# Performance work log

Hardware: AMD Instinct MI355X
Metric: run time of the kernel (lower is better)

The kernel has to match this reference:

```python
import jax, jax.numpy as jnp
import numpy as np

B, T, HID = 2, 2048, 1536
H, HKV, D = 12, 2, 128
EPS = 1e-6
NEG = -1e9


def setup_inputs() -> dict:
    key = jax.random.key(0)
    ks = jax.random.split(key, 8)
    # rotary embeddings built from real angles (cos/sin of position*inv_freq)
    inv_freq = 1.0 / (10000.0 ** (jnp.arange(0, D, 2, dtype=jnp.float32) / D))  # [D/2]
    pos = jnp.arange(T, dtype=jnp.float32)
    ang = pos[:, None] * inv_freq[None, :]                       # [T, D/2]
    emb = jnp.concatenate([ang, ang], axis=-1)                   # [T, D]
    cos = jnp.broadcast_to(jnp.cos(emb)[None], (B, T, D))
    sin = jnp.broadcast_to(jnp.sin(emb)[None], (B, T, D))
    # additive causal mask [1,1,T,T]
    causal = jnp.tril(jnp.ones((T, T), dtype=bool))
    attention_mask = jnp.where(causal, 0.0, NEG).astype(jnp.float32)[None, None]
    s = 0.02
    return {
        "hidden_states": jax.random.normal(ks[0], (B, T, HID), jnp.float32),
        "cos": cos,
        "sin": sin,
        "attention_mask": attention_mask,
        "q_w": jax.random.normal(ks[1], (H * D, HID), jnp.float32) * s,
        "k_w": jax.random.normal(ks[2], (HKV * D, HID), jnp.float32) * s,
        "v_w": jax.random.normal(ks[3], (HKV * D, HID), jnp.float32) * s,
        "o_w": jax.random.normal(ks[4], (HID, H * D), jnp.float32) * s,
        "q_norm_w": jnp.ones((D,), jnp.float32),
        "k_norm_w": jnp.ones((D,), jnp.float32),
    }


def _rms_norm(x, w):
    # per-head RMSNorm over last dim (head_dim), computed in fp32
    xf = x.astype(jnp.float32)
    var = jnp.mean(xf * xf, axis=-1, keepdims=True)
    return (w * (xf * jax.lax.rsqrt(var + EPS))).astype(x.dtype)


def _rotate_half(x):
    x1, x2 = jnp.split(x, 2, axis=-1)
    return jnp.concatenate([-x2, x1], axis=-1)


def reference(hidden_states, cos, sin, attention_mask, q_w, k_w, v_w, o_w, q_norm_w, k_norm_w):
    b, t, _ = hidden_states.shape
    n_rep = H // HKV
    scale = D ** -0.5

    # projections -> [B, n_heads, T, D]
    q = (hidden_states @ q_w.T).reshape(b, t, H, D)
    k = (hidden_states @ k_w.T).reshape(b, t, HKV, D)
    v = (hidden_states @ v_w.T).reshape(b, t, HKV, D).transpose(0, 2, 1, 3)

    # per-head QK RMSNorm, then to [B, H, T, D]
    q = _rms_norm(q, q_norm_w).transpose(0, 2, 1, 3)
    k = _rms_norm(k, k_norm_w).transpose(0, 2, 1, 3)

    # RoPE (cos/sin broadcast over head axis)
    c = cos[:, None, :, :]
    s = sin[:, None, :, :]
    q = q * c + _rotate_half(q) * s
    k = k * c + _rotate_half(k) * s

    # GQA repeat_kv: [B, HKV, T, D] -> [B, H, T, D]
    k = jnp.repeat(k, n_rep, axis=1)
    v = jnp.repeat(v, n_rep, axis=1)

    attn = jnp.einsum('bhqd,bhkd->bhqk', q, k) * scale + attention_mask
    attn = jax.nn.softmax(attn.astype(jnp.float32), axis=-1).astype(q.dtype)
    out = jnp.einsum('bhqk,bhkd->bhqd', attn, v)
    out = out.transpose(0, 2, 1, 3).reshape(b, t, H * D)
    return out @ o_w.T
```

## Files before the change

### kernel.cpp

```cpp
#include <hip/hip_runtime.h>
#include <hip/hip_bf16.h>


#define B_   2
#define T_   2048
#define HID_ 1536
#define H_   12
#define HKV_ 2
#define D_   128
#define GQ_  (H_ / HKV_)
#define NQKV_ 2048
#define SCALE_ 0.08838834764831845f

typedef unsigned short u16;
typedef __attribute__((ext_vector_type(4))) float f32x4;
typedef __attribute__((ext_vector_type(8))) short bf16x8;
typedef __attribute__((ext_vector_type(4))) unsigned short u16x4;
typedef __attribute__((ext_vector_type(8))) unsigned short u16x8;

__device__ __forceinline__ u16 f2b(float f) {
  union { __hip_bfloat16 h; u16 u; } cv;
  cv.h = __float2bfloat16(f);
  return cv.u;
}
__device__ __forceinline__ float b2f(u16 u) {
  union { float f; unsigned i; } cv;
  cv.i = ((unsigned)u) << 16;
  return cv.f;
}

__device__ __forceinline__ void glds16(const u16* g, u16* l) {
  __builtin_amdgcn_global_load_lds((const __attribute__((address_space(1))) void*)g,
                                   (__attribute__((address_space(3))) void*)l, 16, 0, 0);
}

__global__ __launch_bounds__(256) void cvt_f32_bf16(const float* __restrict__ src,
                                                    u16* __restrict__ dst, int n4) {
  int i = blockIdx.x * 256 + threadIdx.x;
  const int stride = gridDim.x * 256;
  for (; i < n4; i += stride) {
    const float4 v = reinterpret_cast<const float4*>(src)[i];
    u16x4 o = {f2b(v.x), f2b(v.y), f2b(v.z), f2b(v.w)};
    reinterpret_cast<u16x4*>(dst)[i] = o;
  }
}

__device__ __forceinline__ void cstore(float* p, float v) { *p = v; }
__device__ __forceinline__ void cstore(u16* p, float v) { *p = f2b(v); }

template <typename CT>
__global__ __launch_bounds__(256) void gemm_bt(const u16* __restrict__ A,
                                               const u16* __restrict__ W,
                                               CT* __restrict__ C,
                                               int M, int N, int K) {
  __shared__ __align__(16) u16 As[128 * 32];
  __shared__ __align__(16) u16 Ws[128 * 32];
  const int tid  = threadIdx.x;
  const int lane = tid & 63;
  const int wid  = tid >> 6;
  const int wr = wid >> 1, wc = wid & 1;
  const int l15 = lane & 15, kg = lane >> 4;
  const int rowBase = blockIdx.y * 128;
  const int colBase = blockIdx.x * 128;

  const int srow = lane >> 2;
  const int scol = (lane & 3) << 3;
  const u16* Ab = A + (size_t)(rowBase + wid * 16 + srow) * K + scol;
  const u16* Wb = W + (size_t)(colBase + wid * 16 + srow) * K + scol;
  u16* AsW = &As[wid * 512];
  u16* WsW = &Ws[wid * 512];

  const f32x4 zero4 = {0.f, 0.f, 0.f, 0.f};
  f32x4 acc[4][4];
#pragma unroll
  for (int m = 0; m < 4; ++m)
#pragma unroll
    for (int n = 0; n < 4; ++n) acc[m][n] = zero4;

  for (int k0 = 0; k0 < K; k0 += 32) {
    __syncthreads();
    glds16(Ab + k0, AsW);
    glds16(Ab + (size_t)64 * K + k0, AsW + 2048);
    glds16(Wb + k0, WsW);
    glds16(Wb + (size_t)64 * K + k0, WsW + 2048);
    __syncthreads();
    bf16x8 a[4], b[4];
#pragma unroll
    for (int m = 0; m < 4; ++m)
      a[m] = *reinterpret_cast<const bf16x8*>(&As[(wr * 64 + m * 16 + l15) * 32 + kg * 8]);
#pragma unroll
    for (int n = 0; n < 4; ++n)
      b[n] = *reinterpret_cast<const bf16x8*>(&Ws[(wc * 64 + n * 16 + l15) * 32 + kg * 8]);
#pragma unroll
    for (int m = 0; m < 4; ++m)
#pragma unroll
      for (int n = 0; n < 4; ++n)
        acc[m][n] = __builtin_amdgcn_mfma_f32_16x16x32_bf16(a[m], b[n], acc[m][n], 0, 0, 0);
  }
#pragma unroll
  for (int m = 0; m < 4; ++m) {
    const int row0 = rowBase + wr * 64 + m * 16 + kg * 4;
#pragma unroll
    for (int n = 0; n < 4; ++n) {
      const int col = colBase + wc * 64 + n * 16 + l15;
#pragma unroll
      for (int r = 0; r < 4; ++r) cstore(&C[(size_t)(row0 + r) * N + col], acc[m][n][r]);
    }
  }
}

__global__ __launch_bounds__(256) void norm_rope_cvt(
    const u16* __restrict__ qkv, const float* __restrict__ cosb,
    const float* __restrict__ sinb, const float* __restrict__ q_nw,
    const float* __restrict__ k_nw, u16* __restrict__ q_b,
    u16* __restrict__ k_b, u16* __restrict__ vt_b) {
  const int gwave = (int)((blockIdx.x * 256 + threadIdx.x) >> 6);
  const int lane = threadIdx.x & 63;
  const int NQ = B_ * T_ * H_;
  const int NK = B_ * T_ * HKV_;
  if (gwave < NQ) {
    const int bt = gwave / H_, h = gwave - bt * H_;
    const u16* src = qkv + (size_t)bt * NQKV_ + h * D_;
    const float x1 = b2f(src[lane]), x2 = b2f(src[lane + 64]);
    float ss = x1 * x1 + x2 * x2;
#pragma unroll
    for (int m = 32; m >= 1; m >>= 1) ss += __shfl_xor(ss, m);
    const float rinv = rsqrtf(ss * (1.0f / D_) + 1e-6f);
    const float c1 = cosb[(size_t)bt * D_ + lane], c2 = cosb[(size_t)bt * D_ + lane + 64];
    const float s1 = sinb[(size_t)bt * D_ + lane], s2 = sinb[(size_t)bt * D_ + lane + 64];
    const float n1 = x1 * rinv * q_nw[lane], n2 = x2 * rinv * q_nw[lane + 64];
    const float o1 = (n1 * c1 - n2 * s1) * SCALE_;
    const float o2 = (n2 * c2 + n1 * s2) * SCALE_;
    const int b = bt >> 11, t = bt & (T_ - 1);
    u16* dst = q_b + ((size_t)(b * H_ + h) * T_ + t) * D_;
    dst[lane] = f2b(o1);
    dst[lane + 64] = f2b(o2);
  } else if (gwave < NQ + NK) {
    const int r = gwave - NQ;
    const int bt = r >> 1, hv = r & 1;
    const u16* src = qkv + (size_t)bt * NQKV_ + 1536 + hv * D_;
    const float x1 = b2f(src[lane]), x2 = b2f(src[lane + 64]);
    float ss = x1 * x1 + x2 * x2;
#pragma unroll
    for (int m = 32; m >= 1; m >>= 1) ss += __shfl_xor(ss, m);
    const float rinv = rsqrtf(ss * (1.0f / D_) + 1e-6f);
    const float c1 = cosb[(size_t)bt * D_ + lane], c2 = cosb[(size_t)bt * D_ + lane + 64];
    const float s1 = sinb[(size_t)bt * D_ + lane], s2 = sinb[(size_t)bt * D_ + lane + 64];
    const float n1 = x1 * rinv * k_nw[lane], n2 = x2 * rinv * k_nw[lane + 64];
    const float o1 = n1 * c1 - n2 * s1;
    const float o2 = n2 * c2 + n1 * s2;
    const int b = bt >> 11, t = bt & (T_ - 1);
    u16* dst = k_b + ((size_t)(b * HKV_ + hv) * T_ + t) * D_;
    dst[lane] = f2b(o1);
    dst[lane + 64] = f2b(o2);
  } else {
    const int r = gwave - NQ - NK;
    const int bt = r >> 1, hv = r & 1;
    const u16* src = qkv + (size_t)bt * NQKV_ + 1792 + hv * D_;
    const float x1 = b2f(src[lane]), x2 = b2f(src[lane + 64]);
    const int b = bt >> 11, t = bt & (T_ - 1);
    u16* dst = vt_b + (size_t)(b * HKV_ + hv) * D_ * T_;
    dst[(size_t)lane * T_ + t] = f2b(x1);
    dst[(size_t)(lane + 64) * T_ + t] = f2b(x2);
  }
}

__global__ __launch_bounds__(256) void attn_kernel(const u16* __restrict__ q_b,
                                                   const u16* __restrict__ k_b,
                                                   const u16* __restrict__ vt_b,
                                                   u16* __restrict__ aout,
                                                   u16* __restrict__ po0,
                                                   float2* __restrict__ ml) {
  __shared__ __align__(16) u16 Ks[64 * 128];
  __shared__ __align__(16) u16 Vs[64 * 128];
  __shared__ __align__(16) u16 P_lds[64][80];
  const int bh = blockIdx.x;
  const int y = blockIdx.y;
  const int qt = (y < 32) ? y : y - 16;
  const int s = (y < 32) ? 0 : 1;
  const int kt0 = s * 16;
  const int ktend = (s == 0) ? min(qt, 15) : qt;
  const bool splitq = (qt >= 16);
  const int b = bh / H_, h = bh - b * H_;
  const int kvh = h / GQ_;
  const int tid = threadIdx.x;
  const int w = tid >> 6, lane = tid & 63;
  const int l15 = lane & 15, kg = lane >> 4;
  const int qbase = qt * 64;

  const u16* Kb = k_b + (size_t)(b * HKV_ + kvh) * T_ * D_;
  const u16* Vb = vt_b + (size_t)(b * HKV_ + kvh) * D_ * T_;

  const u16* qrow = q_b + ((size_t)(b * H_ + h) * T_ + qbase + w * 16 + l15) * D_;
  bf16x8 qf[4];
#pragma unroll
  for (int ss = 0; ss < 4; ++ss)
    qf[ss] = *reinterpret_cast<const bf16x8*>(qrow + ss * 32 + kg * 8);

  const int krow0 = tid >> 4;
  const int kcol8 = (tid & 15) << 3;
  const int kdst0 = krow0 * 128 + (kcol8 ^ (krow0 << 3));
  const u16* ksrc0 = Kb + (size_t)krow0 * D_ + kcol8;

  const int vd0 = tid >> 3;
  const int vkk0 = (tid & 7) << 3;
  const int vdst0 = (vd0 >> 1) * 128 + ((((vd0 & 1) << 6) | vkk0) ^ ((vd0 >> 1) << 3));
  const u16* vsrc0 = Vb + (size_t)vd0 * T_ + vkk0;

  int koff[4];
#pragma unroll
  for (int ss = 0; ss < 4; ++ss) koff[ss] = (ss * 32 + kg * 8) ^ (l15 << 3);
  const int kbase = l15 * 128;
  int voff[2][2];
#pragma unroll
  for (int p = 0; p < 2; ++p)
#pragma unroll
    for (int ks = 0; ks < 2; ++ks)
      voff[p][ks] = (((l15 & 1) << 6) | (ks * 32) | (kg * 8)) ^ (((p << 3) | (l15 >> 1)) << 3);
  const int vrowb = (l15 >> 1) * 128;

  u16x8 kpre[4], vpre[4];
#pragma unroll
  for (int c = 0; c < 4; ++c) {
    kpre[c] = *reinterpret_cast<const u16x8*>(ksrc0 + (size_t)kt0 * 64 * D_ + c * 2048);
    vpre[c] = *reinterpret_cast<const u16x8*>(vsrc0 + (size_t)kt0 * 64 + (size_t)c * 32 * T_);
  }

  const f32x4 zero4 = {0.f, 0.f, 0.f, 0.f};
  f32x4 o[8];
#pragma unroll
  for (int n = 0; n < 8; ++n) o[n] = zero4;
  float mrow[4] = {-3e38f, -3e38f, -3e38f, -3e38f};
  float lsum[4] = {0.f, 0.f, 0.f, 0.f};

  for (int kt = kt0; kt <= ktend; ++kt) {
    __syncthreads();
#pragma unroll
    for (int c = 0; c < 4; ++c) {
      *reinterpret_cast<u16x8*>(&Ks[kdst0 + c * 2048]) = kpre[c];
      *reinterpret_cast<u16x8*>(&Vs[vdst0 + c * 2048]) = vpre[c];
    }
    __syncthreads();
    if (kt < ktend) {
      const size_t kadv = (size_t)(kt + 1) * 64;
#pragma unroll
      for (int c = 0; c < 4; ++c) {
        kpre[c] = *reinterpret_cast<const u16x8*>(ksrc0 + kadv * D_ + c * 2048);
        vpre[c] = *reinterpret_cast<const u16x8*>(vsrc0 + kadv + (size_t)c * 32 * T_);
      }
    }
    f32x4 sc[4];
#pragma unroll
    for (int n = 0; n < 4; ++n) sc[n] = zero4;
#pragma unroll
    for (int n = 0; n < 4; ++n)
#pragma unroll
      for (int ss = 0; ss < 4; ++ss) {
        bf16x8 kf = *reinterpret_cast<const bf16x8*>(&Ks[n * 2048 + kbase + koff[ss]]);
        sc[n] = __builtin_amdgcn_mfma_f32_16x16x32_bf16(qf[ss], kf, sc[n], 0, 0, 0);
      }
    if (kt == qt) {
#pragma unroll
      for (int n = 0; n < 4; ++n)
#pragma unroll
        for (int r = 0; r < 4; ++r)
          if (n * 16 + l15 > w * 16 + kg * 4 + r) sc[n][r] = -3e38f;
    }
    float pmax[4];
#pragma unroll
    for (int r = 0; r < 4; ++r) {
      float v = fmaxf(fmaxf(sc[0][r], sc[1][r]), fmaxf(sc[2][r], sc[3][r]));
      v = fmaxf(v, __shfl_xor(v, 1));
      v = fmaxf(v, __shfl_xor(v, 2));
      v = fmaxf(v, __shfl_xor(v, 4));
      v = fmaxf(v, __shfl_xor(v, 8));
      pmax[r] = v;
    }
    const bool grow = (pmax[0] > mrow[0] + 8.f) | (pmax[1] > mrow[1] + 8.f) |
                      (pmax[2] > mrow[2] + 8.f) | (pmax[3] > mrow[3] + 8.f);
    if (__any(grow)) {
#pragma unroll
      for (int r = 0; r < 4; ++r) {
        const float mnew = fmaxf(mrow[r], pmax[r]);
        const float alpha = __expf(mrow[r] - mnew);
        mrow[r] = mnew;
        lsum[r] *= alpha;
#pragma unroll
        for (int n = 0; n < 8; ++n) o[n][r] *= alpha;
      }
    }
    float rs[4] = {0.f, 0.f, 0.f, 0.f};
#pragma unroll
    for (int n = 0; n < 4; ++n)
#pragma unroll
      for (int r = 0; r < 4; ++r) {
        const float p = __expf(sc[n][r] - mrow[r]);
        rs[r] += p;
        P_lds[w * 16 + kg * 4 + r][n * 16 + l15] = f2b(p);
      }
#pragma unroll
    for (int r = 0; r < 4; ++r) {
      float v = rs[r];
      v += __shfl_xor(v, 1);
      v += __shfl_xor(v, 2);
      v += __shfl_xor(v, 4);
      v += __shfl_xor(v, 8);
      lsum[r] += v;
    }
#pragma unroll
    for (int ks = 0; ks < 2; ++ks) {
      bf16x8 pf = *reinterpret_cast<const bf16x8*>(&P_lds[w * 16 + l15][ks * 32 + kg * 8]);
#pragma unroll
      for (int n = 0; n < 8; ++n) {
        bf16x8 vf = *reinterpret_cast<const bf16x8*>(&Vs[n * 1024 + vrowb + voff[n & 1][ks]]);
        o[n] = __builtin_amdgcn_mfma_f32_16x16x32_bf16(pf, vf, o[n], 0, 0, 0);
      }
    }
  }

  const int t0 = qbase + w * 16 + kg * 4;
  if (!splitq) {
    float inv[4];
#pragma unroll
    for (int r = 0; r < 4; ++r) inv[r] = 1.0f / lsum[r];
#pragma unroll
    for (int n = 0; n < 8; ++n)
#pragma unroll
      for (int r = 0; r < 4; ++r)
        aout[(size_t)(b * T_ + t0 + r) * (H_ * D_) + h * D_ + n * 16 + l15] =
            f2b(o[n][r] * inv[r]);
  } else {
    const int slot = (bh << 4) + (qt - 16);
    if (l15 == 0) {
#pragma unroll
      for (int r = 0; r < 4; ++r) {
        const int row = w * 16 + kg * 4 + r;
        float2 v; v.x = mrow[r]; v.y = lsum[r];
        ml[(size_t)(slot * 2 + s) * 64 + row] = v;
      }
    }
    if (s == 1) {
#pragma unroll
      for (int n = 0; n < 8; ++n)
#pragma unroll
        for (int r = 0; r < 4; ++r)
          aout[(size_t)(b * T_ + t0 + r) * (H_ * D_) + h * D_ + n * 16 + l15] =
              f2b(o[n][r]);
    } else {
#pragma unroll
      for (int n = 0; n < 8; ++n)
#pragma unroll
        for (int r = 0; r < 4; ++r)
          po0[((size_t)slot * 64 + w * 16 + kg * 4 + r) * 128 + n * 16 + l15] =
              f2b(o[n][r]);
    }
  }
}

__global__ __launch_bounds__(256) void combine_kernel(u16* __restrict__ aout,
                                                      const u16* __restrict__ po0,
                                                      const float2* __restrict__ ml) {
  const int bh = blockIdx.x;
  const int qt16 = blockIdx.y;
  const int slot = (bh << 4) + qt16;
  const int b = bh / H_, h = bh - b * H_;
  const int t0 = (qt16 + 16) * 64;
  const int tid = threadIdx.x;
  const int row = tid >> 2;
  const int colc = (tid & 3) << 5;

  const float2 ml0 = ml[(size_t)(slot * 2 + 0) * 64 + row];
  const float2 ml1 = ml[(size_t)(slot * 2 + 1) * 64 + row];
  const float m = fmaxf(ml0.x, ml1.x);
  const float c0 = __expf(ml0.x - m), c1 = __expf(ml1.x - m);
  const float inv = 1.0f / (ml0.y * c0 + ml1.y * c1);
  const float s0 = c0 * inv, s1 = c1 * inv;

  const u16* p0 = po0 + ((size_t)slot * 64 + row) * 128 + colc;
  u16* a = aout + (size_t)(b * T_ + t0 + row) * (H_ * D_) + h * D_ + colc;
#pragma unroll
  for (int j = 0; j < 4; ++j) {
    u16x8 v0 = *reinterpret_cast<const u16x8*>(p0 + j * 8);
    u16x8 v1 = *reinterpret_cast<const u16x8*>(a + j * 8);
    u16x8 out;
#pragma unroll
    for (int e = 0; e < 8; ++e) out[e] = f2b(b2f(v0[e]) * s0 + b2f(v1[e]) * s1);
    *reinterpret_cast<u16x8*>(a + j * 8) = out;
  }
}

extern "C" void kernel_launch(void* const* d_in, const int* in_sizes, int n_in,
                              void* d_out, int out_size, void* d_ws, size_t ws_size,
                              hipStream_t stream) {
  const float* hidden = (const float*)d_in[0];
  const float* cosb   = (const float*)d_in[1];
  const float* sinb   = (const float*)d_in[2];
  const float* q_w  = (const float*)d_in[4];
  const float* k_w  = (const float*)d_in[5];
  const float* v_w  = (const float*)d_in[6];
  const float* o_w  = (const float*)d_in[7];
  const float* q_nw = (const float*)d_in[8];
  const float* k_nw = (const float*)d_in[9];
  float* out = (float*)d_out;

  char* ws = (char*)d_ws;
  const size_t MB = 1u << 20;
  u16*    hidden_b = (u16*)(ws);
  u16*    qkvw     = (u16*)(ws + 12 * MB);
  u16*    q_b      = (u16*)(ws);
  u16*    aout     = (u16*)(ws + 12 * MB);
  float2* ml       = (float2*)(ws + 24 * MB);
  u16*    k_b      = (u16*)(ws + 24 * MB + 512 * 1024);
  u16*    vt_b     = (u16*)(ws + 26 * MB + 512 * 1024);
  u16*    owb      = (u16*)(ws + 28 * MB + 512 * 1024);
  u16*    qkv_proj = (u16*)d_out;
  u16*    po0      = (u16*)d_out;

  const dim3 blk(256);
  const int M = B_ * T_;

  {
    const int nh = (B_ * T_ * HID_) / 4;
    const int nq = (H_ * D_ * HID_) / 4;
    const int nk = (HKV_ * D_ * HID_) / 4;
    cvt_f32_bf16<<<2048, blk, 0, stream>>>(hidden, hidden_b, nh);
    cvt_f32_bf16<<<2048, blk, 0, stream>>>(q_w, qkvw, nq);
    cvt_f32_bf16<<<384, blk, 0, stream>>>(k_w, qkvw + (size_t)1536 * HID_, nk);
    cvt_f32_bf16<<<384, blk, 0, stream>>>(v_w, qkvw + (size_t)1792 * HID_, nk);
    cvt_f32_bf16<<<2048, blk, 0, stream>>>(o_w, owb, nq);
  }

  gemm_bt<u16><<<dim3(NQKV_ / 128, M / 128), blk, 0, stream>>>(hidden_b, qkvw, qkv_proj,
                                                               M, NQKV_, HID_);

  norm_rope_cvt<<<16384, blk, 0, stream>>>(qkv_proj, cosb, sinb, q_nw, k_nw,
                                           q_b, k_b, vt_b);

  attn_kernel<<<dim3(B_ * H_, 48), blk, 0, stream>>>(q_b, k_b, vt_b, aout, po0, ml);
  combine_kernel<<<dim3(B_ * H_, 16), blk, 0, stream>>>(aout, po0, ml);

  gemm_bt<float><<<dim3(HID_ / 128, M / 128), blk, 0, stream>>>(aout, owb, out,
                                                                M, HID_, HID_);
}
```

Before: 216.1 us.

## Restructure attention to 128-row Q tiles with transposed QK and async double-buffered K/V

The attention kernel now processes 128 query rows per block, with each wave holding two 16-row Q sub-tiles, so every K/V fragment read from LDS feeds two MFMAs. S is computed transposed (K as the A operand), which lets P be packed into registers directly and removes the P round-trip through shared memory. K/V tiles are loaded with direct global-to-LDS copies into a double buffer, and V is written in a permuted token order so it matches the MFMA layout. Grid and combine sizes are halved to match. This adds register pressure and lowers the block count, and glds16 must already exist in the hidden part of the code.

```diff
diff --git a/kernel.cpp b/kernel.cpp
--- a/kernel.cpp
+++ b/kernel.cpp
@@ -159,9 +159,12 @@
     const u16* src = qkv + (size_t)bt * NQKV_ + 1792 + hv * D_;
     const float x1 = b2f(src[lane]), x2 = b2f(src[lane + 64]);
     const int b = bt >> 11, t = bt & (T_ - 1);
+    const int kk = t & 63;
+    const int tp = (t & ~63) | (kk & 32) | (((kk >> 2) & 3) << 3) |
+                   (((kk >> 4) & 1) << 2) | (kk & 3);
     u16* dst = vt_b + (size_t)(b * HKV_ + hv) * D_ * T_;
-    dst[(size_t)lane * T_ + t] = f2b(x1);
-    dst[(size_t)(lane + 64) * T_ + t] = f2b(x2);
+    dst[(size_t)lane * T_ + tp] = f2b(x1);
+    dst[(size_t)(lane + 64) * T_ + tp] = f2b(x2);
   }
 }
 
@@ -171,188 +174,227 @@
                                                    u16* __restrict__ aout,
                                                    u16* __restrict__ po0,
                                                    float2* __restrict__ ml) {
-  __shared__ __align__(16) u16 Ks[64 * 128];
-  __shared__ __align__(16) u16 Vs[64 * 128];
-  __shared__ __align__(16) u16 P_lds[64][80];
+  __shared__ __align__(16) u16 Ks[2][64 * 128];
+  __shared__ __align__(16) u16 Vs[2][128 * 64];
   const int bh = blockIdx.x;
   const int y = blockIdx.y;
-  const int qt = (y < 32) ? y : y - 16;
-  const int s = (y < 32) ? 0 : 1;
+  const int qt = (y < 16) ? y : (y - 8);
+  const int s = (y < 16) ? 0 : 1;
   const int kt0 = s * 16;
-  const int ktend = (s == 0) ? min(qt, 15) : qt;
-  const bool splitq = (qt >= 16);
+  const int ktend = (s == 0) ? min(2 * qt + 1, 15) : (2 * qt + 1);
+  const bool splitq = (qt >= 8);
   const int b = bh / H_, h = bh - b * H_;
   const int kvh = h / GQ_;
   const int tid = threadIdx.x;
   const int w = tid >> 6, lane = tid & 63;
   const int l15 = lane & 15, kg = lane >> 4;
-  const int qbase = qt * 64;
+  const int qbase = qt * 128;
 
   const u16* Kb = k_b + (size_t)(b * HKV_ + kvh) * T_ * D_;
   const u16* Vb = vt_b + (size_t)(b * HKV_ + kvh) * D_ * T_;
 
-  const u16* qrow = q_b + ((size_t)(b * H_ + h) * T_ + qbase + w * 16 + l15) * D_;
-  bf16x8 qf[4];
-#pragma unroll
-  for (int ss = 0; ss < 4; ++ss)
-    qf[ss] = *reinterpret_cast<const bf16x8*>(qrow + ss * 32 + kg * 8);
-
-  const int krow0 = tid >> 4;
-  const int kcol8 = (tid & 15) << 3;
-  const int kdst0 = krow0 * 128 + (kcol8 ^ (krow0 << 3));
-  const u16* ksrc0 = Kb + (size_t)krow0 * D_ + kcol8;
-
-  const int vd0 = tid >> 3;
-  const int vkk0 = (tid & 7) << 3;
-  const int vdst0 = (vd0 >> 1) * 128 + ((((vd0 & 1) << 6) | vkk0) ^ ((vd0 >> 1) << 3));
-  const u16* vsrc0 = Vb + (size_t)vd0 * T_ + vkk0;
-
-  int koff[4];
-#pragma unroll
-  for (int ss = 0; ss < 4; ++ss) koff[ss] = (ss * 32 + kg * 8) ^ (l15 << 3);
-  const int kbase = l15 * 128;
-  int voff[2][2];
-#pragma unroll
-  for (int p = 0; p < 2; ++p)
-#pragma unroll
-    for (int ks = 0; ks < 2; ++ks)
-      voff[p][ks] = (((l15 & 1) << 6) | (ks * 32) | (kg * 8)) ^ (((p << 3) | (l15 >> 1)) << 3);
-  const int vrowb = (l15 >> 1) * 128;
-
-  u16x8 kpre[4], vpre[4];
+  bf16x8 qf[2][4];
+#pragma unroll
+  for (int qb = 0; qb < 2; ++qb) {
+    const u16* qrow =
+        q_b + ((size_t)(b * H_ + h) * T_ + qbase + w * 32 + qb * 16 + l15) * D_;
+#pragma unroll
+    for (int s4 = 0; s4 < 4; ++s4)
+      qf[qb][s4] = *reinterpret_cast<const bf16x8*>(qrow + s4 * 32 + kg * 8);
+  }
+
+  int kK[4], vK[4];
 #pragma unroll
   for (int c = 0; c < 4; ++c) {
-    kpre[c] = *reinterpret_cast<const u16x8*>(ksrc0 + (size_t)kt0 * 64 * D_ + c * 2048);
-    vpre[c] = *reinterpret_cast<const u16x8*>(vsrc0 + (size_t)kt0 * 64 + (size_t)c * 32 * T_);
-  }
+    const int ch = w * 4 + c;
+    const int kr = ch * 4 + (lane >> 4);
+    kK[c] = kr * D_ + (((lane & 15) << 3) ^ ((kr & 7) << 3));
+    const int dr = ch * 8 + (lane >> 3);
+    vK[c] = dr * T_ + (((lane & 7) << 3) ^ ((dr & 7) << 3));
+  }
+
+  const int xorv = (l15 & 7) << 3;
 
   const f32x4 zero4 = {0.f, 0.f, 0.f, 0.f};
-  f32x4 o[8];
-#pragma unroll
-  for (int n = 0; n < 8; ++n) o[n] = zero4;
-  float mrow[4] = {-3e38f, -3e38f, -3e38f, -3e38f};
-  float lsum[4] = {0.f, 0.f, 0.f, 0.f};
+  f32x4 o[2][8];
+#pragma unroll
+  for (int qb = 0; qb < 2; ++qb)
+#pragma unroll
+    for (int n = 0; n < 8; ++n) o[qb][n] = zero4;
+  float m[2] = {0.f, 0.f};
+  float lsum[2] = {0.f, 0.f};
+
+  {
+    const size_t kb = (size_t)kt0 * 64;
+#pragma unroll
+    for (int c = 0; c < 4; ++c) {
+      glds16(Kb + kb * D_ + kK[c], &Ks[0][(w * 4 + c) * 512]);
+      glds16(Vb + kb + vK[c], &Vs[0][(w * 4 + c) * 512]);
+    }
+  }
+  __syncthreads();
+  int cur = 0;
 
   for (int kt = kt0; kt <= ktend; ++kt) {
-    __syncthreads();
-#pragma unroll
-    for (int c = 0; c < 4; ++c) {
-      *reinterpret_cast<u16x8*>(&Ks[kdst0 + c * 2048]) = kpre[c];
-      *reinterpret_cast<u16x8*>(&Vs[vdst0 + c * 2048]) = vpre[c];
-    }
-    __syncthreads();
     if (kt < ktend) {
-      const size_t kadv = (size_t)(kt + 1) * 64;
+      const size_t kb = (size_t)(kt + 1) * 64;
 #pragma unroll
       for (int c = 0; c < 4; ++c) {
-        kpre[c] = *reinterpret_cast<const u16x8*>(ksrc0 + kadv * D_ + c * 2048);
-        vpre[c] = *reinterpret_cast<const u16x8*>(vsrc0 + kadv + (size_t)c * 32 * T_);
-      }
-    }
-    f32x4 sc[4];
-#pragma unroll
-    for (int n = 0; n < 4; ++n) sc[n] = zero4;
+        glds16(Kb + kb * D_ + kK[c], &Ks[cur ^ 1][(w * 4 + c) * 512]);
+        glds16(Vb + kb + vK[c], &Vs[cur ^ 1][(w * 4 + c) * 512]);
+      }
+    }
+    f32x4 sc[2][4];
+#pragma unroll
+    for (int qb = 0; qb < 2; ++qb)
+#pragma unroll
+      for (int n = 0; n < 4; ++n) sc[qb][n] = zero4;
 #pragma unroll
     for (int n = 0; n < 4; ++n)
 #pragma unroll
-      for (int ss = 0; ss < 4; ++ss) {
-        bf16x8 kf = *reinterpret_cast<const bf16x8*>(&Ks[n * 2048 + kbase + koff[ss]]);
-        sc[n] = __builtin_amdgcn_mfma_f32_16x16x32_bf16(qf[ss], kf, sc[n], 0, 0, 0);
-      }
-    if (kt == qt) {
+      for (int s4 = 0; s4 < 4; ++s4) {
+        const int koff = (n * 16 + l15) * 128 + ((s4 * 32 + kg * 8) ^ xorv);
+        bf16x8 kf = *reinterpret_cast<const bf16x8*>(&Ks[cur][koff]);
+#pragma unroll
+        for (int qb = 0; qb < 2; ++qb)
+          sc[qb][n] = __builtin_amdgcn_mfma_f32_16x16x32_bf16(kf, qf[qb][s4],
+                                                              sc[qb][n], 0, 0, 0);
+      }
+    if (kt >= 2 * qt) {
+#pragma unroll
+      for (int qb = 0; qb < 2; ++qb) {
+        const int qg = w * 32 + qb * 16 + l15;
+        const int kbb = (kt - 2 * qt) * 64;
+#pragma unroll
+        for (int n = 0; n < 4; ++n)
+#pragma unroll
+          for (int r = 0; r < 4; ++r)
+            if (kbb + n * 16 + kg * 4 + r > qg) sc[qb][n][r] = -3e38f;
+      }
+    }
+    float pm[2];
+#pragma unroll
+    for (int qb = 0; qb < 2; ++qb) {
+      float v = sc[qb][0][0];
 #pragma unroll
       for (int n = 0; n < 4; ++n)
 #pragma unroll
+        for (int r = 0; r < 4; ++r) v = fmaxf(v, sc[qb][n][r]);
+      v = fmaxf(v, __shfl_xor(v, 16));
+      v = fmaxf(v, __shfl_xor(v, 32));
+      pm[qb] = v;
+    }
+    if (__any((pm[0] > m[0] + 8.f) | (pm[1] > m[1] + 8.f))) {
+#pragma unroll
+      for (int qb = 0; qb < 2; ++qb) {
+        const float mn = fmaxf(m[qb], pm[qb]);
+        const float al = __expf(m[qb] - mn);
+        m[qb] = mn;
+        lsum[qb] *= al;
+        float alT[4];
+#pragma unroll
         for (int r = 0; r < 4; ++r)
-          if (n * 16 + l15 > w * 16 + kg * 4 + r) sc[n][r] = -3e38f;
-    }
-    float pmax[4];
-#pragma unroll
-    for (int r = 0; r < 4; ++r) {
-      float v = fmaxf(fmaxf(sc[0][r], sc[1][r]), fmaxf(sc[2][r], sc[3][r]));
-      v = fmaxf(v, __shfl_xor(v, 1));
-      v = fmaxf(v, __shfl_xor(v, 2));
-      v = fmaxf(v, __shfl_xor(v, 4));
-      v = fmaxf(v, __shfl_xor(v, 8));
-      pmax[r] = v;
-    }
-    const bool grow = (pmax[0] > mrow[0] + 8.f) | (pmax[1] > mrow[1] + 8.f) |
-                      (pmax[2] > mrow[2] + 8.f) | (pmax[3] > mrow[3] + 8.f);
-    if (__any(grow)) {
-#pragma unroll
-      for (int r = 0; r < 4; ++r) {
-        const float mnew = fmaxf(mrow[r], pmax[r]);
-        const float alpha = __expf(mrow[r] - mnew);
-        mrow[r] = mnew;
-        lsum[r] *= alpha;
-#pragma unroll
-        for (int n = 0; n < 8; ++n) o[n][r] *= alpha;
-      }
-    }
-    float rs[4] = {0.f, 0.f, 0.f, 0.f};
-#pragma unroll
-    for (int n = 0; n < 4; ++n)
-#pragma unroll
-      for (int r = 0; r < 4; ++r) {
-        const float p = __expf(sc[n][r] - mrow[r]);
-        rs[r] += p;
-        P_lds[w * 16 + kg * 4 + r][n * 16 + l15] = f2b(p);
-      }
-#pragma unroll
-    for (int r = 0; r < 4; ++r) {
-      float v = rs[r];
-      v += __shfl_xor(v, 1);
-      v += __shfl_xor(v, 2);
-      v += __shfl_xor(v, 4);
-      v += __shfl_xor(v, 8);
-      lsum[r] += v;
-    }
-#pragma unroll
-    for (int ks = 0; ks < 2; ++ks) {
-      bf16x8 pf = *reinterpret_cast<const bf16x8*>(&P_lds[w * 16 + l15][ks * 32 + kg * 8]);
-#pragma unroll
-      for (int n = 0; n < 8; ++n) {
-        bf16x8 vf = *reinterpret_cast<const bf16x8*>(&Vs[n * 1024 + vrowb + voff[n & 1][ks]]);
-        o[n] = __builtin_amdgcn_mfma_f32_16x16x32_bf16(pf, vf, o[n], 0, 0, 0);
-      }
-    }
-  }
-
-  const int t0 = qbase + w * 16 + kg * 4;
+          alT[r] = __shfl(al, (lane & 48) | (kg * 4 + r));
+#pragma unroll
+        for (int n = 0; n < 8; ++n)
+#pragma unroll
+          for (int r = 0; r < 4; ++r) o[qb][n][r] *= alT[r];
+      }
+    }
+#pragma unroll
+    for (int qb = 0; qb < 2; ++qb) {
+      float rs = 0.f;
+#pragma unroll
+      for (int n = 0; n < 4; ++n)
+#pragma unroll
+        for (int r = 0; r < 4; ++r) {
+          const float p = __expf(sc[qb][n][r] - m[qb]);
+          sc[qb][n][r] = p;
+          rs += p;
+        }
+      rs += __shfl_xor(rs, 16);
+      rs += __shfl_xor(rs, 32);
+      lsum[qb] += rs;
+    }
+    bf16x8 pf[2][2];
+#pragma unroll
+    for (int qb = 0; qb < 2; ++qb)
+#pragma unroll
+      for (int ks = 0; ks < 2; ++ks)
+#pragma unroll
+        for (int r = 0; r < 4; ++r) {
+          pf[qb][ks][r] = (short)f2b(sc[qb][2 * ks][r]);
+          pf[qb][ks][r + 4] = (short)f2b(sc[qb][2 * ks + 1][r]);
+        }
+#pragma unroll
+    for (int n = 0; n < 8; ++n)
+#pragma unroll
+      for (int ks = 0; ks < 2; ++ks) {
+        const int voff = (n * 16 + l15) * 64 + ((ks * 32 + kg * 8) ^ xorv);
+        bf16x8 vf = *reinterpret_cast<const bf16x8*>(&Vs[cur][voff]);
+#pragma unroll
+        for (int qb = 0; qb < 2; ++qb)
+          o[qb][n] = __builtin_amdgcn_mfma_f32_16x16x32_bf16(pf[qb][ks], vf,
+                                                             o[qb][n], 0, 0, 0);
+      }
+    if (kt < ktend) {
+      __syncthreads();
+      cur ^= 1;
+    }
+  }
+
   if (!splitq) {
-    float inv[4];
-#pragma unroll
-    for (int r = 0; r < 4; ++r) inv[r] = 1.0f / lsum[r];
-#pragma unroll
-    for (int n = 0; n < 8; ++n)
+    float invT[2][4];
+#pragma unroll
+    for (int qb = 0; qb < 2; ++qb) {
+      const float inv = 1.0f / lsum[qb];
 #pragma unroll
       for (int r = 0; r < 4; ++r)
-        aout[(size_t)(b * T_ + t0 + r) * (H_ * D_) + h * D_ + n * 16 + l15] =
-            f2b(o[n][r] * inv[r]);
-  } else {
-    const int slot = (bh << 4) + (qt - 16);
-    if (l15 == 0) {
-#pragma unroll
-      for (int r = 0; r < 4; ++r) {
-        const int row = w * 16 + kg * 4 + r;
-        float2 v; v.x = mrow[r]; v.y = lsum[r];
-        ml[(size_t)(slot * 2 + s) * 64 + row] = v;
-      }
-    }
-    if (s == 1) {
+        invT[qb][r] = __shfl(inv, (lane & 48) | (kg * 4 + r));
+    }
+#pragma unroll
+    for (int qb = 0; qb < 2; ++qb) {
+      const int t0 = qbase + w * 32 + qb * 16 + kg * 4;
 #pragma unroll
       for (int n = 0; n < 8; ++n)
 #pragma unroll
         for (int r = 0; r < 4; ++r)
           aout[(size_t)(b * T_ + t0 + r) * (H_ * D_) + h * D_ + n * 16 + l15] =
-              f2b(o[n][r]);
+              f2b(o[qb][n][r] * invT[qb][r]);
+    }
+  } else {
+    const int slot = bh * 8 + (qt - 8);
+    if (kg == 0) {
+#pragma unroll
+      for (int qb = 0; qb < 2; ++qb) {
+        float2 v;
+        v.x = m[qb];
+        v.y = lsum[qb];
+        ml[(size_t)(slot * 2 + s) * 128 + w * 32 + qb * 16 + l15] = v;
+      }
+    }
+    if (s == 1) {
+#pragma unroll
+      for (int qb = 0; qb < 2; ++qb) {
+        const int t0 = qbase + w * 32 + qb * 16 + kg * 4;
+#pragma unroll
+        for (int n = 0; n < 8; ++n)
+#pragma unroll
+          for (int r = 0; r < 4; ++r)
+            aout[(size_t)(b * T_ + t0 + r) * (H_ * D_) + h * D_ + n * 16 + l15] =
+                f2b(o[qb][n][r]);
+      }
     } else {
 #pragma unroll
-      for (int n = 0; n < 8; ++n)
-#pragma unroll
-        for (int r = 0; r < 4; ++r)
-          po0[((size_t)slot * 64 + w * 16 + kg * 4 + r) * 128 + n * 16 + l15] =
-              f2b(o[n][r]);
+      for (int qb = 0; qb < 2; ++qb) {
+        const int row0 = w * 32 + qb * 16 + kg * 4;
+#pragma unroll
+        for (int n = 0; n < 8; ++n)
+#pragma unroll
+          for (int r = 0; r < 4; ++r)
+            po0[((size_t)slot * 128 + row0 + r) * 128 + n * 16 + l15] =
+                f2b(o[qb][n][r]);
+      }
     }
   }
 }
@@ -361,31 +403,31 @@
                                                       const u16* __restrict__ po0,
                                                       const float2* __restrict__ ml) {
   const int bh = blockIdx.x;
-  const int qt16 = blockIdx.y;
-  const int slot = (bh << 4) + qt16;
+  const int qt8 = blockIdx.y;
+  const int slot = bh * 8 + qt8;
   const int b = bh / H_, h = bh - b * H_;
-  const int t0 = (qt16 + 16) * 64;
+  const int t0 = (qt8 + 8) * 128;
   const int tid = threadIdx.x;
-  const int row = tid >> 2;
-  const int colc = (tid & 3) << 5;
-
-  const float2 ml0 = ml[(size_t)(slot * 2 + 0) * 64 + row];
-  const float2 ml1 = ml[(size_t)(slot * 2 + 1) * 64 + row];
-  const float m = fmaxf(ml0.x, ml1.x);
-  const float c0 = __expf(ml0.x - m), c1 = __expf(ml1.x - m);
+  const int row = tid >> 1;
+  const int colc = (tid & 1) << 6;
+
+  const float2 ml0 = ml[(size_t)(slot * 2 + 0) * 128 + row];
+  const float2 ml1 = ml[(size_t)(slot * 2 + 1) * 128 + row];
+  const float mm = fmaxf(ml0.x, ml1.x);
+  const float c0 = __expf(ml0.x - mm), c1 = __expf(ml1.x - mm);
   const float inv = 1.0f / (ml0.y * c0 + ml1.y * c1);
   const float s0 = c0 * inv, s1 = c1 * inv;
 
-  const u16* p0 = po0 + ((size_t)slot * 64 + row) * 128 + colc;
+  const u16* p0 = po0 + ((size_t)slot * 128 + row) * 128 + colc;
   u16* a = aout + (size_t)(b * T_ + t0 + row) * (H_ * D_) + h * D_ + colc;
 #pragma unroll
-  for (int j = 0; j < 4; ++j) {
+  for (int j = 0; j < 8; ++j) {
     u16x8 v0 = *reinterpret_cast<const u16x8*>(p0 + j * 8);
     u16x8 v1 = *reinterpret_cast<const u16x8*>(a + j * 8);
-    u16x8 out;
-#pragma unroll
-    for (int e = 0; e < 8; ++e) out[e] = f2b(b2f(v0[e]) * s0 + b2f(v1[e]) * s1);
-    *reinterpret_cast<u16x8*>(a + j * 8) = out;
+    u16x8 outv;
+#pragma unroll
+    for (int e = 0; e < 8; ++e) outv[e] = f2b(b2f(v0[e]) * s0 + b2f(v1[e]) * s1);
+    *reinterpret_cast<u16x8*>(a + j * 8) = outv;
   }
 }
 
@@ -436,8 +478,8 @@
   norm_rope_cvt<<<16384, blk, 0, stream>>>(qkv_proj, cosb, sinb, q_nw, k_nw,
                                            q_b, k_b, vt_b);
 
-  attn_kernel<<<dim3(B_ * H_, 48), blk, 0, stream>>>(q_b, k_b, vt_b, aout, po0, ml);
-  combine_kernel<<<dim3(B_ * H_, 16), blk, 0, stream>>>(aout, po0, ml);
+  attn_kernel<<<dim3(B_ * H_, 24), blk, 0, stream>>>(q_b, k_b, vt_b, aout, po0, ml);
+  combine_kernel<<<dim3(B_ * H_, 8), blk, 0, stream>>>(aout, po0, ml);
 
   gemm_bt<float><<<dim3(HID_ / 128, M / 128), blk, 0, stream>>>(aout, owb, out,
                                                                 M, HID_, HID_);
```

Result: faster. 206.5 us (-4.4%).
